# Optimization experiments

Measured on AMD Instinct MI355X. Metric: run time of the kernel, lower is better.

## Reference

```python
import jax, jax.numpy as jnp
import numpy as np

B, C_IN, C_MID, C_OUT, H, W = 256, 2, 128, 64, 15, 15
N_RES = 4  # line_length//2 - 1 with line_length=11

# per-direction input offsets for kernel taps w0 and w2 (w1 is always center),
# matching fix_direction_order=True sparse 3x3 kernel construction:
# dir0 horizontal, dir1 vertical, dir2 anti-diagonal, dir3 main diagonal.
OFFSETS = (((0, -1), (0, 1)),
           ((-1, 0), (1, 0)),
           ((1, -1), (-1, 1)),
           ((-1, -1), (1, 1)))


def shift2d(x, di, dj):
    # out[..., i, j] = x[..., i+di, j+dj] with zero padding (di,dj in {-1,0,1})
    nd = x.ndim
    xp = jnp.pad(x, [(0, 0)] * (nd - 2) + [(1, 1), (1, 1)])
    h, w = x.shape[-2], x.shape[-1]
    return xp[..., 1 + di:1 + di + h, 1 + dj:1 + dj + w]


def dir_conv(x, w, b):
    # x: [4,B,Cin,H,W]; w: [Cout,Cin,3]; b: [Cout]
    x0 = jnp.stack([shift2d(x[d], *OFFSETS[d][0]) for d in range(4)])
    x2 = jnp.stack([shift2d(x[d], *OFFSETS[d][1]) for d in range(4)])
    y = (jnp.einsum('oc,dbchw->dbohw', w[..., 0], x0)
         + jnp.einsum('oc,dbchw->dbohw', w[..., 1], x)
         + jnp.einsum('oc,dbchw->dbohw', w[..., 2], x2))
    return y + b[None, None, :, None, None]


def conv1x1(x, w, b):
    # x: [4,B,Cin,H,W]; w: [Cout,Cin]; b: [Cout]
    return jnp.einsum('oc,dbchw->dbohw', w, x) + b[None, None, :, None, None]


def setup_inputs() -> dict:
    key = jax.random.key(0)
    ks = jax.random.split(key, 16)
    s_in = 1.0 / np.sqrt(3 * C_IN)
    s_mid = 1.0 / np.sqrt(3 * C_MID)
    s_pw = 1.0 / np.sqrt(C_MID)
    return {
        'x': jax.random.normal(ks[0], (B, C_IN, H, W), jnp.float32),
        'dconv0_w': jax.random.normal(ks[1], (C_MID, C_IN, 3), jnp.float32) * s_in,
        'dconv0_b': jnp.zeros((C_MID,), jnp.float32),
        'res_dconv_w': jax.random.normal(ks[2], (N_RES, C_MID, C_MID, 3), jnp.float32) * s_mid,
        'res_dconv_b': jnp.zeros((N_RES, C_MID), jnp.float32),
        'res_pw_w': jax.random.normal(ks[3], (N_RES, C_MID, C_MID), jnp.float32) * s_pw,
        'res_pw_b': jnp.zeros((N_RES, C_MID), jnp.float32),
        'c0_w1': jax.random.normal(ks[4], (C_MID, C_MID), jnp.float32) * s_pw,
        'c0_b1': jnp.zeros((C_MID,), jnp.float32),
        'c0_w2': jax.random.normal(ks[5], (C_MID, C_MID), jnp.float32) * s_pw,
        'c0_b2': jnp.zeros((C_MID,), jnp.float32),
        'final_w': jax.random.normal(ks[6], (C_OUT, C_MID), jnp.float32) * s_pw,
        'final_b': jnp.zeros((C_OUT,), jnp.float32),
    }


def reference(x, dconv0_w, dconv0_b, res_dconv_w, res_dconv_b,
              res_pw_w, res_pw_b, c0_w1, c0_b1, c0_w2, c0_b2,
              final_w, final_b):
    act = jax.nn.silu
    # all 4 direction streams start from the same input plane
    h = jnp.broadcast_to(x[None], (4,) + x.shape)  # [4,B,Cin,H,W]
    h = act(dir_conv(h, dconv0_w, dconv0_b))
    # DirectionalConvResBlocks (norm='none')
    for i in range(N_RES):
        r = h
        h = act(dir_conv(h, res_dconv_w[i], res_dconv_b[i]))
        h = act(conv1x1(h, res_pw_w[i], res_pw_b[i]))
        h = h + r
    # Conv0dResBlock (two 1x1 convs, middle_dim_multipler=1)
    r = h
    h = act(conv1x1(h, c0_w1, c0_b1))
    h = act(conv1x1(h, c0_w2, c0_b2))
    h = h + r
    # final 1x1 conv, then stack directions at dim=1 -> [B,4,Cout,H,W]
    h = conv1x1(h, final_w, final_b)
    return jnp.transpose(h, (1, 0, 2, 3, 4))
```

## Files before the change

### kernel.cpp

```cpp
#include <hip/hip_runtime.h>

using u16 = unsigned short;
using u32 = unsigned int;

typedef __bf16 bf16x8 __attribute__((ext_vector_type(8)));
typedef float  f32x4  __attribute__((ext_vector_type(4)));

#define NPOS   225
#define NT     15
#define ROWP   136
#define A_ROWS 289
#define B_ROWS 241
#define A_ELEMS (A_ROWS*ROWP)
#define B_ELEMS (B_ROWS*ROWP)
#define LDS_BYTES ((A_ELEMS + B_ELEMS)*2)
#define RSTRIDE17 (17*ROWP)

#define WA_PER_L 49152
#define WP_OFF   (4*WA_PER_L)
#define WP_PER   16384
#define WF_OFF   (WP_OFF + 6*WP_PER)
#define W_U16_TOTAL (WF_OFF + 8192)

__host__ __device__ __forceinline__ int permc(int c){
  return (c & ~0x3C) | (((c >> 2) & 3) << 4) | (((c >> 4) & 3) << 2);
}

__device__ __forceinline__ float bflo(u32 q){ return __uint_as_float(q << 16); }
__device__ __forceinline__ float bfhi(u32 q){ return __uint_as_float(q & 0xffff0000u); }
__device__ __forceinline__ u16 f2bf(float f){
  u32 u = __float_as_uint(f);
  return (u16)((u + 0x7fffu + ((u >> 16) & 1u)) >> 16);
}
__device__ __forceinline__ u32 packbf(float a, float b){
  union { __bf16 h[2]; u32 u; } r;
  r.h[0] = (__bf16)a; r.h[1] = (__bf16)b;
  return r.u;
}
__device__ __forceinline__ float silu_f(float x){
  return x * __builtin_amdgcn_rcpf(1.f + __expf(-x));
}
__device__ __forceinline__ f32x4 mfma16(bf16x8 a, bf16x8 b, f32x4 c){
  return __builtin_amdgcn_mfma_f32_16x16x32_bf16(a, b, c, 0, 0, 0);
}

__global__ void prep_w(const float* __restrict__ d0w, const float* __restrict__ d0b,
                       const float* __restrict__ rdw,
                       const float* __restrict__ rpw, const float* __restrict__ c1w,
                       const float* __restrict__ c2w, const float* __restrict__ fw,
                       float* __restrict__ ws)
{
  u16* wsb = (u16*)(ws + 896);
  const int total = 896 + W_U16_TOTAL;
  for (int idx = blockIdx.x*blockDim.x + threadIdx.x; idx < total; idx += gridDim.x*blockDim.x){
    if (idx < 768){
      int k = idx >> 7, s = idx & 127;
      ws[idx] = d0w[permc(s)*6 + k];
      continue;
    }
    if (idx < 896){
      int s = idx - 768;
      ws[idx] = d0b[permc(s)];
      continue;
    }
    int e = idx - 896;
    float v;
    if (e < WP_OFF){
      int L = e / WA_PER_L, r = e % WA_PER_L;
      int og = r / 24576; int r1 = r - og*24576;
      int tap = r1 >> 13; int r2 = r1 & 8191;
      int ot = r2 >> 11, kb = (r2 >> 9) & 3, l = (r2 >> 3) & 63, j = r2 & 7;
      int o = (og*4 + ot)*16 + (l & 15);
      int ks = kb*32 + ((l >> 4) << 3) + j;
      v = rdw[((L*128 + o)*128 + permc(ks))*3 + tap];
    } else if (e < WF_OFF){
      int t2 = e - WP_OFF;
      int i = t2 / WP_PER, r = t2 % WP_PER;
      int og2 = r >> 13;
      int ot = (r >> 11) & 3, kb = (r >> 9) & 3, l = (r >> 3) & 63, j = r & 7;
      int o = (og2*4 + ot)*16 + (l & 15);
      int ks = kb*32 + ((l >> 4) << 3) + j;
      v = (i < 4) ? rpw[(i*128 + o)*128 + permc(ks)]
        : (i == 4) ? c1w[o*128 + permc(ks)] : c2w[o*128 + permc(ks)];
    } else {
      int e2 = e - WF_OFF;
      int ot = e2 >> 11, kb = (e2 >> 9) & 3, l = (e2 >> 3) & 63, j = e2 & 7;
      int o = ot*16 + (l & 15);
      int ks = kb*32 + ((l >> 4) << 3) + j;
      v = fw[o*128 + permc(ks)];
    }
    wsb[e] = f2bf(v);
  }
}

__device__ __forceinline__ uint4 pack_silu2(const f32x4& a, const f32x4& b){
  uint4 q;
  q.x = packbf(silu_f(a[0]), silu_f(a[1]));
  q.y = packbf(silu_f(a[2]), silu_f(a[3]));
  q.z = packbf(silu_f(b[0]), silu_f(b[1]));
  q.w = packbf(silu_f(b[2]), silu_f(b[3]));
  return q;
}

template<int NTL>
__device__ __forceinline__ void dconv_mfma(const u16* __restrict__ As, u16* __restrict__ Bs,
    const u16* __restrict__ wloc, const float* __restrict__ bias,
    int lane, int og, int T0, int off0, int off2)
{
  const int col = lane & 15, kg = lane >> 4, koff = kg*8;
  f32x4 acc[4][NTL];
  #pragma unroll
  for (int ot=0; ot<4; ++ot){
    f32x4 bz = *(const f32x4*)(bias + og*64 + ot*16 + kg*4);
    #pragma unroll
    for (int t=0;t<NTL;++t) acc[ot][t] = bz;
  }
  const int c1 = (col+1)*ROWP + koff;
  #pragma unroll 1
  for (int tap=0; tap<3; ++tap){
    const int offr = (tap==0) ? off0 : (tap==1) ? 0 : off2;
    bf16x8 w[4][4];
    #pragma unroll
    for (int ot=0; ot<4; ++ot)
      #pragma unroll
      for (int kb=0; kb<4; ++kb)
        w[ot][kb] = *(const bf16x8*)(wloc + tap*8192 + ot*2048 + kb*512 + lane*8);
    #pragma unroll
    for (int t=0; t<NTL; ++t){
      const u16* s = As + (T0+t+1)*RSTRIDE17 + c1 + offr;
      __builtin_amdgcn_s_setprio(1);
      #pragma unroll
      for (int kb=0; kb<4; ++kb){
        bf16x8 v = *(const bf16x8*)(s + kb*32);
        acc[0][t] = mfma16(w[0][kb], v, acc[0][t]);
        acc[1][t] = mfma16(w[1][kb], v, acc[1][t]);
        acc[2][t] = mfma16(w[2][kb], v, acc[2][t]);
        acc[3][t] = mfma16(w[3][kb], v, acc[3][t]);
      }
      __builtin_amdgcn_s_setprio(0);
    }
  }
  if (col < 15){
    #pragma unroll
    for (int t=0;t<NTL;++t){
      u16* dp = Bs + ((T0+t)*16+col)*ROWP + og*64 + kg*16;
      uint4 q0 = pack_silu2(acc[0][t], acc[1][t]);
      uint4 q1 = pack_silu2(acc[2][t], acc[3][t]);
      *(uint4*)dp = q0;
      *(uint4*)(dp+8) = q1;
    }
  }
}

template<bool SRC_HALO, bool DST_HALO, bool RESID>
__device__ __forceinline__ void pw_mfma(const u16* __restrict__ src, u16* __restrict__ dst,
    const u16* __restrict__ wloc, const float* __restrict__ bias,
    int lane, int og2, int T0, int T1)
{
  const int col = lane & 15, kg = lane >> 4, koff = kg*8;
  bf16x8 wp[4][4];
  #pragma unroll
  for (int ot=0; ot<4; ++ot)
    #pragma unroll
    for (int kb=0; kb<4; ++kb)
      wp[ot][kb] = *(const bf16x8*)(wloc + og2*8192 + ot*2048 + kb*512 + lane*8);
  f32x4 bz[4];
  #pragma unroll
  for (int ot=0; ot<4; ++ot) bz[ot] = *(const f32x4*)(bias + og2*64 + ot*16 + kg*4);
  const int c1 = (col+1)*ROWP;
  #pragma unroll 2
  for (int tile=T0; tile<T1; ++tile){
    const int rh = (tile+1)*RSTRIDE17 + c1;
    const int rc = (tile*16+col)*ROWP;
    const u16* S = src + (SRC_HALO ? rh : rc) + koff;
    f32x4 a0 = bz[0], a1 = bz[1], a2 = bz[2], a3 = bz[3];
    __builtin_amdgcn_s_setprio(1);
    #pragma unroll
    for (int kb=0; kb<4; ++kb){
      bf16x8 v = *(const bf16x8*)(S + kb*32);
      a0 = mfma16(wp[0][kb], v, a0);
      a1 = mfma16(wp[1][kb], v, a1);
      a2 = mfma16(wp[2][kb], v, a2);
      a3 = mfma16(wp[3][kb], v, a3);
    }
    __builtin_amdgcn_s_setprio(0);
    if (col < 15){
      u16* dp = dst + (DST_HALO ? rh : rc) + og2*64 + kg*16;
      float s0 = silu_f(a0[0]), s1 = silu_f(a0[1]), s2 = silu_f(a0[2]), s3 = silu_f(a0[3]);
      float s4 = silu_f(a1[0]), s5 = silu_f(a1[1]), s6 = silu_f(a1[2]), s7 = silu_f(a1[3]);
      float s8 = silu_f(a2[0]), s9 = silu_f(a2[1]), sa = silu_f(a2[2]), sb = silu_f(a2[3]);
      float sc = silu_f(a3[0]), sd = silu_f(a3[1]), se = silu_f(a3[2]), sf = silu_f(a3[3]);
      if (RESID){
        uint4 r0 = *(const uint4*)dp;
        uint4 r1 = *(const uint4*)(dp+8);
        s0 += bflo(r0.x); s1 += bfhi(r0.x); s2 += bflo(r0.y); s3 += bfhi(r0.y);
        s4 += bflo(r0.z); s5 += bfhi(r0.z); s6 += bflo(r0.w); s7 += bfhi(r0.w);
        s8 += bflo(r1.x); s9 += bfhi(r1.x); sa += bflo(r1.y); sb += bfhi(r1.y);
        sc += bflo(r1.z); sd += bfhi(r1.z); se += bflo(r1.w); sf += bfhi(r1.w);
      }
      uint4 q0, q1;
      q0.x = packbf(s0, s1); q0.y = packbf(s2, s3);
      q0.z = packbf(s4, s5); q0.w = packbf(s6, s7);
      q1.x = packbf(s8, s9); q1.y = packbf(sa, sb);
      q1.z = packbf(sc, sd); q1.w = packbf(se, sf);
      *(uint4*)dp = q0;
      *(uint4*)(dp+8) = q1;
    }
  }
}

__device__ __forceinline__ void fin_mfma(const u16* __restrict__ As,
    const u16* __restrict__ wloc, const float* __restrict__ bias,
    float* __restrict__ out, int lane, int ogf, int T0, int T1, int bd)
{
  const int col = lane & 15, kg = lane >> 4, koff = kg*8;
  bf16x8 wf[2][4];
  #pragma unroll
  for (int ot=0; ot<2; ++ot)
    #pragma unroll
    for (int kb=0; kb<4; ++kb)
      wf[ot][kb] = *(const bf16x8*)(wloc + (ogf*2+ot)*2048 + kb*512 + lane*8);
  f32x4 bz0 = *(const f32x4*)(bias + ogf*32 + kg*4);
  f32x4 bz1 = *(const f32x4*)(bias + ogf*32 + 16 + kg*4);
  const int c1 = (col+1)*ROWP;
  #pragma unroll 1
  for (int tile=T0; tile<T1; ++tile){
    const u16* S = As + (tile+1)*RSTRIDE17 + c1 + koff;
    f32x4 a0 = bz0, a1 = bz1;
    __builtin_amdgcn_s_setprio(1);
    #pragma unroll
    for (int kb=0; kb<4; ++kb){
      bf16x8 v = *(const bf16x8*)(S + kb*32);
      a0 = mfma16(wf[0][kb], v, a0);
      a1 = mfma16(wf[1][kb], v, a1);
    }
    __builtin_amdgcn_s_setprio(0);
    if (col < 15){
      float* op = out + ((size_t)(bd*64 + ogf*32 + kg*4))*NPOS + tile*15 + col;
      op[0]      = a0[0];
      op[NPOS]   = a0[1];
      op[2*NPOS] = a0[2];
      op[3*NPOS] = a0[3];
      float* oq = op + 16*NPOS;
      oq[0]      = a1[0];
      oq[NPOS]   = a1[1];
      oq[2*NPOS] = a1[2];
      oq[3*NPOS] = a1[3];
    }
  }
}

__global__ void __launch_bounds__(512, 2)
mix9_main(const float* __restrict__ x,
          const float* __restrict__ b_rd,
          const float* __restrict__ b_rp,
          const float* __restrict__ b_c1,
          const float* __restrict__ b_c2,
          const float* __restrict__ b_fin,
          const float* __restrict__ wt,
          float* __restrict__ out)
{
  extern __shared__ u16 sm[];
  u16* As = sm;
  u16* Bs = sm + A_ELEMS;

  const int blk  = blockIdx.x;
  const int b    = blk >> 2, d = blk & 3;
  const int tid  = threadIdx.x;
  const int wave = __builtin_amdgcn_readfirstlane(tid >> 6);
  const int lane = tid & 63;

  const int ogd  = wave >> 2;
  const int pgd  = wave & 3;
  const int og2  = wave >> 2;
  const int ph4  = wave & 3;
  const int T0p  = ph4 * 4;
  const int T1p  = (ph4 == 3) ? NT : T0p + 4;
  const int ob   = wave * 16;

  const int DI0[4] = {0,-1, 1,-1}, DJ0[4] = {-1, 0,-1,-1};
  const int DI2[4] = {0, 1,-1, 1}, DJ2[4] = { 1, 0, 1, 1};
  const int di0 = DI0[d], dj0 = DJ0[d], di2 = DI2[d], dj2 = DJ2[d];
  const int off0 = (di0*17 + dj0)*ROWP;
  const int off2 = (di2*17 + dj2)*ROWP;

  for (int k2 = tid; k2 < A_ELEMS; k2 += 512) As[k2] = 0;
  float* xs = (float*)Bs;
  for (int k2 = tid; k2 < 2*NPOS; k2 += 512) xs[k2] = x[b*(2*NPOS) + k2];
  __syncthreads();

  const float* b0p = wt + 768;
  #pragma unroll 1
  for (int pb = 0; pb < 4; ++pb){
    int pp = pb*64 + lane;
    int i = pp >> 4, j = pp & 15;
    if (i >= 15 || j >= 15) continue;
    float acc[16];
    #pragma unroll
    for (int oo=0;oo<16;++oo) acc[oo] = b0p[ob+oo];
    #pragma unroll
    for (int c=0;c<2;++c){
      int i0=i+di0, j0=j+dj0, i2=i+di2, j2=j+dj2;
      float x0 = ((unsigned)i0<15u && (unsigned)j0<15u) ? xs[c*NPOS + i0*15 + j0] : 0.f;
      float x1 = xs[c*NPOS + i*15 + j];
      float x2 = ((unsigned)i2<15u && (unsigned)j2<15u) ? xs[c*NPOS + i2*15 + j2] : 0.f;
      const float* w0r = wt + (c*3+0)*128 + ob;
      const float* w1r = wt + (c*3+1)*128 + ob;
      const float* w2r = wt + (c*3+2)*128 + ob;
      #pragma unroll
      for (int oo=0;oo<16;++oo)
        acc[oo] = fmaf(w0r[oo],x0, fmaf(w1r[oo],x1, fmaf(w2r[oo],x2, acc[oo])));
    }
    u16* dp = As + ((i+1)*17 + (j+1))*ROWP + ob;
    #pragma unroll
    for (int oo=0;oo<16;oo+=2)
      *(u32*)(dp+oo) = packbf(silu_f(acc[oo]), silu_f(acc[oo+1]));
  }
  __syncthreads();

  const u16* wsb = (const u16*)(wt + 896);

  #pragma unroll 1
  for (int L = 0; L < 4; ++L){
    if (pgd == 3)
      dconv_mfma<3>(As, Bs, wsb + L*WA_PER_L + ogd*24576, b_rd + L*128, lane, ogd, 12, off0, off2);
    else
      dconv_mfma<4>(As, Bs, wsb + L*WA_PER_L + ogd*24576, b_rd + L*128, lane, ogd, pgd*4, off0, off2);
    __syncthreads();
    pw_mfma<false,true,true>(Bs, As, wsb + WP_OFF + L*WP_PER, b_rp + L*128, lane, og2, T0p, T1p);
    __syncthreads();
  }

  pw_mfma<true,false,false>(As, Bs, wsb + WP_OFF + 4*WP_PER, b_c1, lane, og2, T0p, T1p);
  __syncthreads();
  pw_mfma<false,true,true>(Bs, As, wsb + WP_OFF + 5*WP_PER, b_c2, lane, og2, T0p, T1p);
  __syncthreads();

  fin_mfma(As, wsb + WF_OFF, b_fin, out, lane, og2, T0p, T1p, b*4 + d);
}

extern "C" void kernel_launch(void* const* d_in, const int* in_sizes, int n_in,
                              void* d_out, int out_size, void* d_ws, size_t ws_size,
                              hipStream_t stream)
{
  const float* x     = (const float*)d_in[0];
  const float* w_d0  = (const float*)d_in[1];
  const float* b_d0  = (const float*)d_in[2];
  const float* w_rd  = (const float*)d_in[3];
  const float* b_rd  = (const float*)d_in[4];
  const float* w_rp  = (const float*)d_in[5];
  const float* b_rp  = (const float*)d_in[6];
  const float* w_c1  = (const float*)d_in[7];
  const float* b_c1  = (const float*)d_in[8];
  const float* w_c2  = (const float*)d_in[9];
  const float* b_c2  = (const float*)d_in[10];
  const float* w_fin = (const float*)d_in[11];
  const float* b_fin = (const float*)d_in[12];
  float* wt  = (float*)d_ws;
  float* out = (float*)d_out;

  prep_w<<<128, 512, 0, stream>>>(w_d0, b_d0, w_rd, w_rp, w_c1, w_c2, w_fin, wt);

  (void)hipFuncSetAttribute((const void*)mix9_main,
                            hipFuncAttributeMaxDynamicSharedMemorySize, LDS_BYTES);
  mix9_main<<<1024, 512, LDS_BYTES, stream>>>(x, b_rd, b_rp, b_c1, b_c2, b_fin, wt, out);
}
```

Before: 243.5 us.

## Split work by spatial row tiles per wave, drop second LDS buffer

Each wave now owns a pair of spatial rows and computes all 128 output channels, instead of splitting waves across output-channel groups and row groups. The pointwise, residual and tail 1x1 convs then run in place on the owning wave's rows, so the B buffer, several block barriers and the separate fin kernel stage are removed. Weight layouts in the prep kernel are reordered to match the new per-kb, 8-output-tile access pattern. The cost is more accumulator registers (8x2 tiles), weights loaded from global per kb inside loops, and uneven load because the last wave gets a single row.

```diff
diff --git a/kernel.cpp b/kernel.cpp
--- a/kernel.cpp
+++ b/kernel.cpp
@@ -10,10 +10,8 @@
 #define NT     15
 #define ROWP   136
 #define A_ROWS 289
-#define B_ROWS 241
 #define A_ELEMS (A_ROWS*ROWP)
-#define B_ELEMS (B_ROWS*ROWP)
-#define LDS_BYTES ((A_ELEMS + B_ELEMS)*2)
+#define LDS_BYTES ((A_ELEMS + 1024)*2)
 #define RSTRIDE17 (17*ROWP)
 
 #define WA_PER_L 49152
@@ -42,6 +40,22 @@
 }
 __device__ __forceinline__ f32x4 mfma16(bf16x8 a, bf16x8 b, f32x4 c){
   return __builtin_amdgcn_mfma_f32_16x16x32_bf16(a, b, c, 0, 0, 0);
+}
+__device__ __forceinline__ uint4 pack_silu2(const f32x4& a, const f32x4& b){
+  uint4 q;
+  q.x = packbf(silu_f(a[0]), silu_f(a[1]));
+  q.y = packbf(silu_f(a[2]), silu_f(a[3]));
+  q.z = packbf(silu_f(b[0]), silu_f(b[1]));
+  q.w = packbf(silu_f(b[2]), silu_f(b[3]));
+  return q;
+}
+__device__ __forceinline__ uint4 silu_add4(const f32x4& a, const f32x4& b, const uint4& r){
+  uint4 q;
+  q.x = packbf(silu_f(a[0]) + bflo(r.x), silu_f(a[1]) + bfhi(r.x));
+  q.y = packbf(silu_f(a[2]) + bflo(r.y), silu_f(a[3]) + bfhi(r.y));
+  q.z = packbf(silu_f(b[0]) + bflo(r.z), silu_f(b[1]) + bfhi(r.z));
+  q.w = packbf(silu_f(b[2]) + bflo(r.w), silu_f(b[3]) + bfhi(r.w));
+  return q;
 }
 
 __global__ void prep_w(const float* __restrict__ d0w, const float* __restrict__ d0b,
@@ -67,24 +81,22 @@
     float v;
     if (e < WP_OFF){
       int L = e / WA_PER_L, r = e % WA_PER_L;
-      int og = r / 24576; int r1 = r - og*24576;
-      int tap = r1 >> 13; int r2 = r1 & 8191;
-      int ot = r2 >> 11, kb = (r2 >> 9) & 3, l = (r2 >> 3) & 63, j = r2 & 7;
-      int o = (og*4 + ot)*16 + (l & 15);
+      int tap = r / 16384, r1 = r % 16384;
+      int kb = r1 >> 12, ot = (r1 >> 9) & 7, l = (r1 >> 3) & 63, j = r1 & 7;
+      int o = ot*16 + (l & 15);
       int ks = kb*32 + ((l >> 4) << 3) + j;
       v = rdw[((L*128 + o)*128 + permc(ks))*3 + tap];
     } else if (e < WF_OFF){
       int t2 = e - WP_OFF;
       int i = t2 / WP_PER, r = t2 % WP_PER;
-      int og2 = r >> 13;
-      int ot = (r >> 11) & 3, kb = (r >> 9) & 3, l = (r >> 3) & 63, j = r & 7;
-      int o = (og2*4 + ot)*16 + (l & 15);
+      int kb = r >> 12, ot = (r >> 9) & 7, l = (r >> 3) & 63, j = r & 7;
+      int o = ot*16 + (l & 15);
       int ks = kb*32 + ((l >> 4) << 3) + j;
       v = (i < 4) ? rpw[(i*128 + o)*128 + permc(ks)]
         : (i == 4) ? c1w[o*128 + permc(ks)] : c2w[o*128 + permc(ks)];
     } else {
       int e2 = e - WF_OFF;
-      int ot = e2 >> 11, kb = (e2 >> 9) & 3, l = (e2 >> 3) & 63, j = e2 & 7;
+      int kb = e2 >> 11, ot = (e2 >> 9) & 3, l = (e2 >> 3) & 63, j = e2 & 7;
       int o = ot*16 + (l & 15);
       int ks = kb*32 + ((l >> 4) << 3) + j;
       v = fw[o*128 + permc(ks)];
@@ -93,159 +105,202 @@
   }
 }
 
-__device__ __forceinline__ uint4 pack_silu2(const f32x4& a, const f32x4& b){
-  uint4 q;
-  q.x = packbf(silu_f(a[0]), silu_f(a[1]));
-  q.y = packbf(silu_f(a[2]), silu_f(a[3]));
-  q.z = packbf(silu_f(b[0]), silu_f(b[1]));
-  q.w = packbf(silu_f(b[2]), silu_f(b[3]));
-  return q;
-}
-
 template<int NTL>
-__device__ __forceinline__ void dconv_mfma(const u16* __restrict__ As, u16* __restrict__ Bs,
-    const u16* __restrict__ wloc, const float* __restrict__ bias,
-    int lane, int og, int T0, int off0, int off2)
-{
-  const int col = lane & 15, kg = lane >> 4, koff = kg*8;
-  f32x4 acc[4][NTL];
-  #pragma unroll
-  for (int ot=0; ot<4; ++ot){
-    f32x4 bz = *(const f32x4*)(bias + og*64 + ot*16 + kg*4);
+__device__ __forceinline__ void dconv_phase(f32x4 (&acc)[8][2],
+    const u16* __restrict__ As, const u16* __restrict__ wd,
+    const float* __restrict__ bd, int lane, int T0, int dr0, int dr2)
+{
+  const int col = lane & 15, kg = lane >> 4;
+  #pragma unroll
+  for (int ot=0; ot<8; ++ot){
+    f32x4 bz = *(const f32x4*)(bd + ot*16 + kg*4);
     #pragma unroll
     for (int t=0;t<NTL;++t) acc[ot][t] = bz;
   }
-  const int c1 = (col+1)*ROWP + koff;
+  const int rb0 = ((T0+1)*17 + col + 1)*ROWP + kg*8;
   #pragma unroll 1
   for (int tap=0; tap<3; ++tap){
-    const int offr = (tap==0) ? off0 : (tap==1) ? 0 : off2;
-    bf16x8 w[4][4];
+    const int offr = ((tap==0) ? dr0 : (tap==1) ? 0 : dr2)*ROWP;
+    #pragma unroll 1
+    for (int kb=0; kb<4; ++kb){
+      bf16x8 w[8];
+      #pragma unroll
+      for (int ot=0; ot<8; ++ot)
+        w[ot] = *(const bf16x8*)(wd + ((tap*4+kb)*8 + ot)*512 + lane*8);
+      #pragma unroll
+      for (int t=0; t<NTL; ++t){
+        bf16x8 v = *(const bf16x8*)(As + rb0 + offr + t*RSTRIDE17 + kb*32);
+        __builtin_amdgcn_s_setprio(1);
+        acc[0][t] = mfma16(w[0], v, acc[0][t]);
+        acc[1][t] = mfma16(w[1], v, acc[1][t]);
+        acc[2][t] = mfma16(w[2], v, acc[2][t]);
+        acc[3][t] = mfma16(w[3], v, acc[3][t]);
+        acc[4][t] = mfma16(w[4], v, acc[4][t]);
+        acc[5][t] = mfma16(w[5], v, acc[5][t]);
+        acc[6][t] = mfma16(w[6], v, acc[6][t]);
+        acc[7][t] = mfma16(w[7], v, acc[7][t]);
+        __builtin_amdgcn_s_setprio(0);
+      }
+    }
+  }
+}
+
+template<int NTL>
+__device__ __forceinline__ void pwres_phase(f32x4 (&acc)[8][2],
+    u16* __restrict__ As, const u16* __restrict__ wpw,
+    const float* __restrict__ bp, int lane, int T0)
+{
+  const int col = lane & 15, kg = lane >> 4;
+  const int rb0 = ((T0+1)*17 + col + 1)*ROWP;
+  uint4 rsd[NTL][4];
+  #pragma unroll
+  for (int t=0;t<NTL;++t){
+    const u16* rp = As + rb0 + t*RSTRIDE17 + kg*16;
+    rsd[t][0] = *(const uint4*)rp;
+    rsd[t][1] = *(const uint4*)(rp + 8);
+    rsd[t][2] = *(const uint4*)(rp + 64);
+    rsd[t][3] = *(const uint4*)(rp + 72);
+  }
+  #pragma unroll
+  for (int t=0;t<NTL;++t){
+    if (col < 15){
+      u16* dp = As + rb0 + t*RSTRIDE17 + kg*16;
+      *(uint4*)dp      = pack_silu2(acc[0][t], acc[1][t]);
+      *(uint4*)(dp+8)  = pack_silu2(acc[2][t], acc[3][t]);
+      *(uint4*)(dp+64) = pack_silu2(acc[4][t], acc[5][t]);
+      *(uint4*)(dp+72) = pack_silu2(acc[6][t], acc[7][t]);
+    }
+  }
+  #pragma unroll
+  for (int t=0;t<NTL;++t){
+    f32x4 a[8];
     #pragma unroll
-    for (int ot=0; ot<4; ++ot)
-      #pragma unroll
-      for (int kb=0; kb<4; ++kb)
-        w[ot][kb] = *(const bf16x8*)(wloc + tap*8192 + ot*2048 + kb*512 + lane*8);
+    for (int ot=0;ot<8;++ot) a[ot] = *(const f32x4*)(bp + ot*16 + kg*4);
+    const u16* srow = As + rb0 + t*RSTRIDE17 + kg*8;
+    #pragma unroll 1
+    for (int kb=0; kb<4; ++kb){
+      bf16x8 w[8];
+      #pragma unroll
+      for (int ot=0; ot<8; ++ot)
+        w[ot] = *(const bf16x8*)(wpw + (kb*8 + ot)*512 + lane*8);
+      bf16x8 v = *(const bf16x8*)(srow + kb*32);
+      __builtin_amdgcn_s_setprio(1);
+      a[0] = mfma16(w[0], v, a[0]); a[1] = mfma16(w[1], v, a[1]);
+      a[2] = mfma16(w[2], v, a[2]); a[3] = mfma16(w[3], v, a[3]);
+      a[4] = mfma16(w[4], v, a[4]); a[5] = mfma16(w[5], v, a[5]);
+      a[6] = mfma16(w[6], v, a[6]); a[7] = mfma16(w[7], v, a[7]);
+      __builtin_amdgcn_s_setprio(0);
+    }
+    if (col < 15){
+      u16* dp = As + rb0 + t*RSTRIDE17 + kg*16;
+      *(uint4*)dp      = silu_add4(a[0], a[1], rsd[t][0]);
+      *(uint4*)(dp+8)  = silu_add4(a[2], a[3], rsd[t][1]);
+      *(uint4*)(dp+64) = silu_add4(a[4], a[5], rsd[t][2]);
+      *(uint4*)(dp+72) = silu_add4(a[6], a[7], rsd[t][3]);
+    }
+  }
+}
+
+template<int NTL>
+__device__ __forceinline__ void tail_phase(u16* __restrict__ As,
+    const u16* __restrict__ w1, const u16* __restrict__ w2, const u16* __restrict__ wf,
+    const float* __restrict__ b1, const float* __restrict__ b2, const float* __restrict__ bf,
+    float* __restrict__ out, int lane, int T0, int bd)
+{
+  const int col = lane & 15, kg = lane >> 4;
+  const int rb0 = ((T0+1)*17 + col + 1)*ROWP;
+  uint4 rsd[NTL][4];
+  #pragma unroll
+  for (int t=0;t<NTL;++t){
+    const u16* rp = As + rb0 + t*RSTRIDE17 + kg*16;
+    rsd[t][0] = *(const uint4*)rp;
+    rsd[t][1] = *(const uint4*)(rp + 8);
+    rsd[t][2] = *(const uint4*)(rp + 64);
+    rsd[t][3] = *(const uint4*)(rp + 72);
+  }
+  #pragma unroll
+  for (int t=0;t<NTL;++t){
+    f32x4 a[8];
     #pragma unroll
-    for (int t=0; t<NTL; ++t){
-      const u16* s = As + (T0+t+1)*RSTRIDE17 + c1 + offr;
+    for (int ot=0;ot<8;++ot) a[ot] = *(const f32x4*)(b1 + ot*16 + kg*4);
+    const u16* srow = As + rb0 + t*RSTRIDE17 + kg*8;
+    #pragma unroll 1
+    for (int kb=0; kb<4; ++kb){
+      bf16x8 w[8];
+      #pragma unroll
+      for (int ot=0; ot<8; ++ot)
+        w[ot] = *(const bf16x8*)(w1 + (kb*8 + ot)*512 + lane*8);
+      bf16x8 v = *(const bf16x8*)(srow + kb*32);
       __builtin_amdgcn_s_setprio(1);
-      #pragma unroll
-      for (int kb=0; kb<4; ++kb){
-        bf16x8 v = *(const bf16x8*)(s + kb*32);
-        acc[0][t] = mfma16(w[0][kb], v, acc[0][t]);
-        acc[1][t] = mfma16(w[1][kb], v, acc[1][t]);
-        acc[2][t] = mfma16(w[2][kb], v, acc[2][t]);
-        acc[3][t] = mfma16(w[3][kb], v, acc[3][t]);
+      a[0] = mfma16(w[0], v, a[0]); a[1] = mfma16(w[1], v, a[1]);
+      a[2] = mfma16(w[2], v, a[2]); a[3] = mfma16(w[3], v, a[3]);
+      a[4] = mfma16(w[4], v, a[4]); a[5] = mfma16(w[5], v, a[5]);
+      a[6] = mfma16(w[6], v, a[6]); a[7] = mfma16(w[7], v, a[7]);
+      __builtin_amdgcn_s_setprio(0);
+    }
+    if (col < 15){
+      u16* dp = As + rb0 + t*RSTRIDE17 + kg*16;
+      *(uint4*)dp      = pack_silu2(a[0], a[1]);
+      *(uint4*)(dp+8)  = pack_silu2(a[2], a[3]);
+      *(uint4*)(dp+64) = pack_silu2(a[4], a[5]);
+      *(uint4*)(dp+72) = pack_silu2(a[6], a[7]);
+    }
+  }
+  #pragma unroll
+  for (int t=0;t<NTL;++t){
+    f32x4 a[8];
+    #pragma unroll
+    for (int ot=0;ot<8;++ot) a[ot] = *(const f32x4*)(b2 + ot*16 + kg*4);
+    const u16* srow = As + rb0 + t*RSTRIDE17 + kg*8;
+    #pragma unroll 1
+    for (int kb=0; kb<4; ++kb){
+      bf16x8 w[8];
+      #pragma unroll
+      for (int ot=0; ot<8; ++ot)
+        w[ot] = *(const bf16x8*)(w2 + (kb*8 + ot)*512 + lane*8);
+      bf16x8 v = *(const bf16x8*)(srow + kb*32);
+      __builtin_amdgcn_s_setprio(1);
+      a[0] = mfma16(w[0], v, a[0]); a[1] = mfma16(w[1], v, a[1]);
+      a[2] = mfma16(w[2], v, a[2]); a[3] = mfma16(w[3], v, a[3]);
+      a[4] = mfma16(w[4], v, a[4]); a[5] = mfma16(w[5], v, a[5]);
+      a[6] = mfma16(w[6], v, a[6]); a[7] = mfma16(w[7], v, a[7]);
+      __builtin_amdgcn_s_setprio(0);
+    }
+    if (col < 15){
+      u16* dp = As + rb0 + t*RSTRIDE17 + kg*16;
+      *(uint4*)dp      = silu_add4(a[0], a[1], rsd[t][0]);
+      *(uint4*)(dp+8)  = silu_add4(a[2], a[3], rsd[t][1]);
+      *(uint4*)(dp+64) = silu_add4(a[4], a[5], rsd[t][2]);
+      *(uint4*)(dp+72) = silu_add4(a[6], a[7], rsd[t][3]);
+    }
+  }
+  #pragma unroll
+  for (int t=0;t<NTL;++t){
+    f32x4 a4[4];
+    #pragma unroll
+    for (int ot=0;ot<4;++ot) a4[ot] = *(const f32x4*)(bf + ot*16 + kg*4);
+    const u16* srow = As + rb0 + t*RSTRIDE17 + kg*8;
+    #pragma unroll 1
+    for (int kb=0; kb<4; ++kb){
+      bf16x8 w[4];
+      #pragma unroll
+      for (int ot=0; ot<4; ++ot)
+        w[ot] = *(const bf16x8*)(wf + (kb*4 + ot)*512 + lane*8);
+      bf16x8 v = *(const bf16x8*)(srow + kb*32);
+      __builtin_amdgcn_s_setprio(1);
+      a4[0] = mfma16(w[0], v, a4[0]); a4[1] = mfma16(w[1], v, a4[1]);
+      a4[2] = mfma16(w[2], v, a4[2]); a4[3] = mfma16(w[3], v, a4[3]);
+      __builtin_amdgcn_s_setprio(0);
+    }
+    if (col < 15){
+      #pragma unroll
+      for (int ot=0; ot<4; ++ot){
+        float* op = out + ((size_t)(bd*64 + ot*16 + kg*4))*NPOS + (T0+t)*15 + col;
+        op[0]      = a4[ot][0];
+        op[NPOS]   = a4[ot][1];
+        op[2*NPOS] = a4[ot][2];
+        op[3*NPOS] = a4[ot][3];
       }
-      __builtin_amdgcn_s_setprio(0);
-    }
-  }
-  if (col < 15){
-    #pragma unroll
-    for (int t=0;t<NTL;++t){
-      u16* dp = Bs + ((T0+t)*16+col)*ROWP + og*64 + kg*16;
-      uint4 q0 = pack_silu2(acc[0][t], acc[1][t]);
-      uint4 q1 = pack_silu2(acc[2][t], acc[3][t]);
-      *(uint4*)dp = q0;
-      *(uint4*)(dp+8) = q1;
-    }
-  }
-}
-
-template<bool SRC_HALO, bool DST_HALO, bool RESID>
-__device__ __forceinline__ void pw_mfma(const u16* __restrict__ src, u16* __restrict__ dst,
-    const u16* __restrict__ wloc, const float* __restrict__ bias,
-    int lane, int og2, int T0, int T1)
-{
-  const int col = lane & 15, kg = lane >> 4, koff = kg*8;
-  bf16x8 wp[4][4];
-  #pragma unroll
-  for (int ot=0; ot<4; ++ot)
-    #pragma unroll
-    for (int kb=0; kb<4; ++kb)
-      wp[ot][kb] = *(const bf16x8*)(wloc + og2*8192 + ot*2048 + kb*512 + lane*8);
-  f32x4 bz[4];
-  #pragma unroll
-  for (int ot=0; ot<4; ++ot) bz[ot] = *(const f32x4*)(bias + og2*64 + ot*16 + kg*4);
-  const int c1 = (col+1)*ROWP;
-  #pragma unroll 2
-  for (int tile=T0; tile<T1; ++tile){
-    const int rh = (tile+1)*RSTRIDE17 + c1;
-    const int rc = (tile*16+col)*ROWP;
-    const u16* S = src + (SRC_HALO ? rh : rc) + koff;
-    f32x4 a0 = bz[0], a1 = bz[1], a2 = bz[2], a3 = bz[3];
-    __builtin_amdgcn_s_setprio(1);
-    #pragma unroll
-    for (int kb=0; kb<4; ++kb){
-      bf16x8 v = *(const bf16x8*)(S + kb*32);
-      a0 = mfma16(wp[0][kb], v, a0);
-      a1 = mfma16(wp[1][kb], v, a1);
-      a2 = mfma16(wp[2][kb], v, a2);
-      a3 = mfma16(wp[3][kb], v, a3);
-    }
-    __builtin_amdgcn_s_setprio(0);
-    if (col < 15){
-      u16* dp = dst + (DST_HALO ? rh : rc) + og2*64 + kg*16;
-      float s0 = silu_f(a0[0]), s1 = silu_f(a0[1]), s2 = silu_f(a0[2]), s3 = silu_f(a0[3]);
-      float s4 = silu_f(a1[0]), s5 = silu_f(a1[1]), s6 = silu_f(a1[2]), s7 = silu_f(a1[3]);
-      float s8 = silu_f(a2[0]), s9 = silu_f(a2[1]), sa = silu_f(a2[2]), sb = silu_f(a2[3]);
-      float sc = silu_f(a3[0]), sd = silu_f(a3[1]), se = silu_f(a3[2]), sf = silu_f(a3[3]);
-      if (RESID){
-        uint4 r0 = *(const uint4*)dp;
-        uint4 r1 = *(const uint4*)(dp+8);
-        s0 += bflo(r0.x); s1 += bfhi(r0.x); s2 += bflo(r0.y); s3 += bfhi(r0.y);
-        s4 += bflo(r0.z); s5 += bfhi(r0.z); s6 += bflo(r0.w); s7 += bfhi(r0.w);
-        s8 += bflo(r1.x); s9 += bfhi(r1.x); sa += bflo(r1.y); sb += bfhi(r1.y);
-        sc += bflo(r1.z); sd += bfhi(r1.z); se += bflo(r1.w); sf += bfhi(r1.w);
-      }
-      uint4 q0, q1;
-      q0.x = packbf(s0, s1); q0.y = packbf(s2, s3);
-      q0.z = packbf(s4, s5); q0.w = packbf(s6, s7);
-      q1.x = packbf(s8, s9); q1.y = packbf(sa, sb);
-      q1.z = packbf(sc, sd); q1.w = packbf(se, sf);
-      *(uint4*)dp = q0;
-      *(uint4*)(dp+8) = q1;
-    }
-  }
-}
-
-__device__ __forceinline__ void fin_mfma(const u16* __restrict__ As,
-    const u16* __restrict__ wloc, const float* __restrict__ bias,
-    float* __restrict__ out, int lane, int ogf, int T0, int T1, int bd)
-{
-  const int col = lane & 15, kg = lane >> 4, koff = kg*8;
-  bf16x8 wf[2][4];
-  #pragma unroll
-  for (int ot=0; ot<2; ++ot)
-    #pragma unroll
-    for (int kb=0; kb<4; ++kb)
-      wf[ot][kb] = *(const bf16x8*)(wloc + (ogf*2+ot)*2048 + kb*512 + lane*8);
-  f32x4 bz0 = *(const f32x4*)(bias + ogf*32 + kg*4);
-  f32x4 bz1 = *(const f32x4*)(bias + ogf*32 + 16 + kg*4);
-  const int c1 = (col+1)*ROWP;
-  #pragma unroll 1
-  for (int tile=T0; tile<T1; ++tile){
-    const u16* S = As + (tile+1)*RSTRIDE17 + c1 + koff;
-    f32x4 a0 = bz0, a1 = bz1;
-    __builtin_amdgcn_s_setprio(1);
-    #pragma unroll
-    for (int kb=0; kb<4; ++kb){
-      bf16x8 v = *(const bf16x8*)(S + kb*32);
-      a0 = mfma16(wf[0][kb], v, a0);
-      a1 = mfma16(wf[1][kb], v, a1);
-    }
-    __builtin_amdgcn_s_setprio(0);
-    if (col < 15){
-      float* op = out + ((size_t)(bd*64 + ogf*32 + kg*4))*NPOS + tile*15 + col;
-      op[0]      = a0[0];
-      op[NPOS]   = a0[1];
-      op[2*NPOS] = a0[2];
-      op[3*NPOS] = a0[3];
-      float* oq = op + 16*NPOS;
-      oq[0]      = a1[0];
-      oq[NPOS]   = a1[1];
-      oq[2*NPOS] = a1[2];
-      oq[3*NPOS] = a1[3];
     }
   }
 }
@@ -262,81 +317,76 @@
 {
   extern __shared__ u16 sm[];
   u16* As = sm;
-  u16* Bs = sm + A_ELEMS;
 
   const int blk  = blockIdx.x;
   const int b    = blk >> 2, d = blk & 3;
   const int tid  = threadIdx.x;
   const int wave = __builtin_amdgcn_readfirstlane(tid >> 6);
   const int lane = tid & 63;
-
-  const int ogd  = wave >> 2;
-  const int pgd  = wave & 3;
-  const int og2  = wave >> 2;
-  const int ph4  = wave & 3;
-  const int T0p  = ph4 * 4;
-  const int T1p  = (ph4 == 3) ? NT : T0p + 4;
-  const int ob   = wave * 16;
+  const int T0   = 2*wave;
 
   const int DI0[4] = {0,-1, 1,-1}, DJ0[4] = {-1, 0,-1,-1};
   const int DI2[4] = {0, 1,-1, 1}, DJ2[4] = { 1, 0, 1, 1};
   const int di0 = DI0[d], dj0 = DJ0[d], di2 = DI2[d], dj2 = DJ2[d];
-  const int off0 = (di0*17 + dj0)*ROWP;
-  const int off2 = (di2*17 + dj2)*ROWP;
+  const int dr0 = di0*17 + dj0;
+  const int dr2 = di2*17 + dj2;
 
   for (int k2 = tid; k2 < A_ELEMS; k2 += 512) As[k2] = 0;
-  float* xs = (float*)Bs;
-  for (int k2 = tid; k2 < 2*NPOS; k2 += 512) xs[k2] = x[b*(2*NPOS) + k2];
+  float* xs = (float*)(As + A_ELEMS);
+  if (tid < 450) xs[tid] = x[b*450 + tid];
   __syncthreads();
 
-  const float* b0p = wt + 768;
-  #pragma unroll 1
-  for (int pb = 0; pb < 4; ++pb){
-    int pp = pb*64 + lane;
-    int i = pp >> 4, j = pp & 15;
-    if (i >= 15 || j >= 15) continue;
-    float acc[16];
-    #pragma unroll
-    for (int oo=0;oo<16;++oo) acc[oo] = b0p[ob+oo];
-    #pragma unroll
-    for (int c=0;c<2;++c){
-      int i0=i+di0, j0=j+dj0, i2=i+di2, j2=j+dj2;
-      float x0 = ((unsigned)i0<15u && (unsigned)j0<15u) ? xs[c*NPOS + i0*15 + j0] : 0.f;
-      float x1 = xs[c*NPOS + i*15 + j];
-      float x2 = ((unsigned)i2<15u && (unsigned)j2<15u) ? xs[c*NPOS + i2*15 + j2] : 0.f;
-      const float* w0r = wt + (c*3+0)*128 + ob;
-      const float* w1r = wt + (c*3+1)*128 + ob;
-      const float* w2r = wt + (c*3+2)*128 + ob;
-      #pragma unroll
-      for (int oo=0;oo<16;++oo)
-        acc[oo] = fmaf(w0r[oo],x0, fmaf(w1r[oo],x1, fmaf(w2r[oo],x2, acc[oo])));
-    }
-    u16* dp = As + ((i+1)*17 + (j+1))*ROWP + ob;
-    #pragma unroll
-    for (int oo=0;oo<16;oo+=2)
-      *(u32*)(dp+oo) = packbf(silu_f(acc[oo]), silu_f(acc[oo+1]));
+  {
+    const float* b0p = wt + 768;
+    const int ob = wave * 16;
+    #pragma unroll 1
+    for (int pb = 0; pb < 4; ++pb){
+      int pp = pb*64 + lane;
+      int i = pp >> 4, j = pp & 15;
+      if (i >= 15 || j >= 15) continue;
+      float acc0[16];
+      #pragma unroll
+      for (int oo=0;oo<16;++oo) acc0[oo] = b0p[ob+oo];
+      #pragma unroll
+      for (int c=0;c<2;++c){
+        int i0=i+di0, j0=j+dj0, i2=i+di2, j2=j+dj2;
+        float x0 = ((unsigned)i0<15u && (unsigned)j0<15u) ? xs[c*NPOS + i0*15 + j0] : 0.f;
+        float x1 = xs[c*NPOS + i*15 + j];
+        float x2 = ((unsigned)i2<15u && (unsigned)j2<15u) ? xs[c*NPOS + i2*15 + j2] : 0.f;
+        const float* w0r = wt + (c*3+0)*128 + ob;
+        const float* w1r = wt + (c*3+1)*128 + ob;
+        const float* w2r = wt + (c*3+2)*128 + ob;
+        #pragma unroll
+        for (int oo=0;oo<16;++oo)
+          acc0[oo] = fmaf(w0r[oo],x0, fmaf(w1r[oo],x1, fmaf(w2r[oo],x2, acc0[oo])));
+      }
+      u16* dp = As + ((i+1)*17 + (j+1))*ROWP + ob;
+      #pragma unroll
+      for (int oo=0;oo<16;oo+=2)
+        *(u32*)(dp+oo) = packbf(silu_f(acc0[oo]), silu_f(acc0[oo+1]));
+    }
   }
   __syncthreads();
 
   const u16* wsb = (const u16*)(wt + 896);
+  f32x4 acc[8][2];
 
   #pragma unroll 1
   for (int L = 0; L < 4; ++L){
-    if (pgd == 3)
-      dconv_mfma<3>(As, Bs, wsb + L*WA_PER_L + ogd*24576, b_rd + L*128, lane, ogd, 12, off0, off2);
-    else
-      dconv_mfma<4>(As, Bs, wsb + L*WA_PER_L + ogd*24576, b_rd + L*128, lane, ogd, pgd*4, off0, off2);
+    if (wave < 7) dconv_phase<2>(acc, As, wsb + L*WA_PER_L, b_rd + L*128, lane, T0, dr0, dr2);
+    else          dconv_phase<1>(acc, As, wsb + L*WA_PER_L, b_rd + L*128, lane, 14, dr0, dr2);
     __syncthreads();
-    pw_mfma<false,true,true>(Bs, As, wsb + WP_OFF + L*WP_PER, b_rp + L*128, lane, og2, T0p, T1p);
-    __syncthreads();
-  }
-
-  pw_mfma<true,false,false>(As, Bs, wsb + WP_OFF + 4*WP_PER, b_c1, lane, og2, T0p, T1p);
-  __syncthreads();
-  pw_mfma<false,true,true>(Bs, As, wsb + WP_OFF + 5*WP_PER, b_c2, lane, og2, T0p, T1p);
-  __syncthreads();
-
-  fin_mfma(As, wsb + WF_OFF, b_fin, out, lane, og2, T0p, T1p, b*4 + d);
+    if (wave < 7) pwres_phase<2>(acc, As, wsb + WP_OFF + L*WP_PER, b_rp + L*128, lane, T0);
+    else          pwres_phase<1>(acc, As, wsb + WP_OFF + L*WP_PER, b_rp + L*128, lane, 14);
+    if (L < 3) __syncthreads();
+  }
+
+  if (wave < 7)
+    tail_phase<2>(As, wsb + WP_OFF + 4*WP_PER, wsb + WP_OFF + 5*WP_PER, wsb + WF_OFF,
+                  b_c1, b_c2, b_fin, out, lane, T0, b*4 + d);
+  else
+    tail_phase<1>(As, wsb + WP_OFF + 4*WP_PER, wsb + WP_OFF + 5*WP_PER, wsb + WF_OFF,
+                  b_c1, b_c2, b_fin, out, lane, 14, b*4 + d);
 }
 
 extern "C" void kernel_launch(void* const* d_in, const int* in_sizes, int n_in,
```

New measurement: 285.9 us. 17.4% more time.
